# Performance work log

Hardware: AMD Instinct MI355X
Metric: run time of the kernel (lower is better)

The kernel has to match this reference:

```python
import jax, jax.numpy as jnp
import numpy as np

N_NODES = 100000
FEAT_DIM = 128
EMBED_DIM = 128
NUM_SAMPLE = 10


def setup_inputs() -> dict:
    key = jax.random.key(0)
    k1, k2, k3, k4, k5 = jax.random.split(key, 5)
    features = jax.random.normal(k1, (N_NODES, FEAT_DIM), dtype=jnp.float32)
    W1 = jax.random.normal(k2, (EMBED_DIM, FEAT_DIM), dtype=jnp.float32) * (1.0 / np.sqrt(FEAT_DIM))
    W2 = jax.random.normal(k3, (EMBED_DIM, EMBED_DIM), dtype=jnp.float32) * (1.0 / np.sqrt(EMBED_DIM))
    adj = jax.random.randint(k4, (N_NODES, NUM_SAMPLE), 0, N_NODES, dtype=jnp.int64)
    nodes = jax.random.randint(k5, (N_NODES,), 0, N_NODES, dtype=jnp.int64)
    return {"features": features, "W1": W1, "W2": W2, "adj": adj, "nodes": nodes}


def reference(features, W1, W2, adj, nodes):
    # 2-layer GraphSAGE with gcn=True: mean over {self} U sampled neighbors,
    # then relu(agg @ W.T). Layer 1 is computed for all nodes since layer 2
    # needs embeddings of arbitrary neighbors.
    n = features.shape[0]
    self_idx = jnp.arange(n, dtype=adj.dtype)[:, None]            # [N,1]
    neigh1 = jnp.concatenate([self_idx, adj], axis=1)             # [N,S+1]
    agg1 = jnp.mean(features[neigh1], axis=1)                     # [N,F] (gather+mean)
    h1 = jax.nn.relu(agg1 @ W1.T)                                 # [N,E]

    neigh2 = jnp.concatenate([nodes[:, None], adj[nodes]], axis=1)  # [B,S+1]
    agg2 = jnp.mean(h1[neigh2], axis=1)                           # [B,E]
    out = jax.nn.relu(agg2 @ W2.T).T                              # [E,B], Encoder returns embed_dim x num_nodes
    return out
```

## Files before the change

kernel.cpp:

```cpp
#include <hip/hip_runtime.h>

#define N_NODES 100000
#define DIM 128
#define NS 10
#define SCALE (1.0f / 11.0f)

typedef unsigned int uint;
typedef unsigned short ushort;
typedef __attribute__((ext_vector_type(8))) short bf16x8;
typedef __attribute__((ext_vector_type(4))) float f32x4;

__device__ inline float bl(uint u) {
    union { uint x; float f; } c; c.x = u << 16; return c.f;
}
__device__ inline uint f2b(float x) {
    union { float f; uint u; } c; c.f = x;
    return (c.u + 0x7FFFu + ((c.u >> 16) & 1u)) >> 16;
}

__global__ __launch_bounds__(256) void wsplit(const float* __restrict__ W1,
                                              const float* __restrict__ W2,
                                              ushort* __restrict__ o) {
    const int i = blockIdx.x * 256 + threadIdx.x;
    const float a = W1[i];
    uint h = f2b(a);
    o[i] = (ushort)h;
    o[16384 + i] = (ushort)f2b(a - bl(h));
    const float b = W2[i];
    h = f2b(b);
    o[32768 + i] = (ushort)h;
    o[49152 + i] = (ushort)f2b(b - bl(h));
}

__global__ __launch_bounds__(256, 2) void gemm1(const float* __restrict__ X,
                                                const ushort* __restrict__ Whi,
                                                const ushort* __restrict__ Wlo,
                                                ushort* __restrict__ C) {
    __shared__ __align__(16) ushort lds[8192];
    const int t = threadIdx.x;
    const int lane = t & 63;
    const int wave = t >> 6;
    const int m16 = lane & 15;
    const int kq = lane >> 4;
    const int r0 = blockIdx.x * 32;

    const int v0 = t, v1 = t + 256;
    const int ln0 = v0 & 63, ln1 = v1 & 63;
    const float* s0 = X + (size_t)(r0 + (v0 >> 8) * 16 + (ln0 & 15)) * DIM +
                      ((v0 >> 6) & 3) * 32 + (ln0 >> 4) * 8;
    const float* s1 = X + (size_t)(r0 + (v1 >> 8) * 16 + (ln1 & 15)) * DIM +
                      ((v1 >> 6) & 3) * 32 + (ln1 >> 4) * 8;
    const float4 f00 = *(const float4*)(s0);
    const float4 f01 = *(const float4*)(s0 + 4);
    const float4 f10 = *(const float4*)(s1);
    const float4 f11 = *(const float4*)(s1 + 4);

    bf16x8 wh[2][4], wl[2][4];
#pragma unroll
    for (int c = 0; c < 2; ++c)
#pragma unroll
        for (int ks = 0; ks < 4; ++ks) {
            const size_t off = (size_t)((2 * wave + c) * 16 + m16) * DIM + ks * 32 + kq * 8;
            wh[c][ks] = *(const bf16x8*)(Whi + off);
            wl[c][ks] = *(const bf16x8*)(Wlo + off);
        }

    {
        const float xs[8] = {f00.x, f00.y, f00.z, f00.w, f01.x, f01.y, f01.z, f01.w};
        bf16x8 hi, lo;
#pragma unroll
        for (int j = 0; j < 8; ++j) {
            const uint hb = f2b(xs[j]);
            hi[j] = (short)hb;
            lo[j] = (short)f2b(xs[j] - bl(hb));
        }
        *(bf16x8*)(lds + (v0 >> 6) * 512 + ln0 * 8) = hi;
        *(bf16x8*)(lds + 4096 + (v0 >> 6) * 512 + ln0 * 8) = lo;
    }
    {
        const float xs[8] = {f10.x, f10.y, f10.z, f10.w, f11.x, f11.y, f11.z, f11.w};
        bf16x8 hi, lo;
#pragma unroll
        for (int j = 0; j < 8; ++j) {
            const uint hb = f2b(xs[j]);
            hi[j] = (short)hb;
            lo[j] = (short)f2b(xs[j] - bl(hb));
        }
        *(bf16x8*)(lds + (v1 >> 6) * 512 + ln1 * 8) = hi;
        *(bf16x8*)(lds + 4096 + (v1 >> 6) * 512 + ln1 * 8) = lo;
    }
    __syncthreads();

    f32x4 acc[2][2];
#pragma unroll
    for (int bt = 0; bt < 2; ++bt)
#pragma unroll
        for (int c = 0; c < 2; ++c) acc[bt][c] = (f32x4){0.f, 0.f, 0.f, 0.f};

#pragma unroll
    for (int ks = 0; ks < 4; ++ks) {
#pragma unroll
        for (int bt = 0; bt < 2; ++bt) {
            const int g = bt * 4 + ks;
            const bf16x8 xh = *(const bf16x8*)(lds + g * 512 + lane * 8);
            const bf16x8 xl = *(const bf16x8*)(lds + 4096 + g * 512 + lane * 8);
#pragma unroll
            for (int c = 0; c < 2; ++c) {
                acc[bt][c] = __builtin_amdgcn_mfma_f32_16x16x32_bf16(wh[c][ks], xh, acc[bt][c], 0, 0, 0);
                acc[bt][c] = __builtin_amdgcn_mfma_f32_16x16x32_bf16(wl[c][ks], xh, acc[bt][c], 0, 0, 0);
                acc[bt][c] = __builtin_amdgcn_mfma_f32_16x16x32_bf16(wh[c][ks], xl, acc[bt][c], 0, 0, 0);
            }
        }
    }

#pragma unroll
    for (int bt = 0; bt < 2; ++bt) {
        const size_t row = (size_t)(r0 + bt * 16 + m16);
#pragma unroll
        for (int c = 0; c < 2; ++c) {
            uint2 w;
            w.x = f2b(acc[bt][c][0]) | (f2b(acc[bt][c][1]) << 16);
            w.y = f2b(acc[bt][c][2]) | (f2b(acc[bt][c][3]) << 16);
            *(uint2*)(C + row * DIM + (2 * wave + c) * 16 + kq * 4) = w;
        }
    }
}

__global__ __launch_bounds__(256, 2) void gemm2t(const ushort* __restrict__ P,
                                                 const ushort* __restrict__ Whi,
                                                 const ushort* __restrict__ Wlo,
                                                 float* __restrict__ out) {
    __shared__ __align__(16) ushort lds[4096];
    const int t = threadIdx.x;
    const int lane = t & 63;
    const int wave = t >> 6;
    const int m16 = lane & 15;
    const int kq = lane >> 4;
    const int r0 = blockIdx.x * 32;

    const int v0 = t, v1 = t + 256;
    const int ln0 = v0 & 63, ln1 = v1 & 63;
    const ushort* s0 = P + (size_t)(r0 + (v0 >> 8) * 16 + (ln0 & 15)) * DIM +
                       ((v0 >> 6) & 3) * 32 + (ln0 >> 4) * 8;
    const ushort* s1 = P + (size_t)(r0 + (v1 >> 8) * 16 + (ln1 & 15)) * DIM +
                       ((v1 >> 6) & 3) * 32 + (ln1 >> 4) * 8;
    const bf16x8 p0 = *(const bf16x8*)(s0);
    const bf16x8 p1 = *(const bf16x8*)(s1);

    bf16x8 wh[2][4], wl[2][4];
#pragma unroll
    for (int c = 0; c < 2; ++c)
#pragma unroll
        for (int ks = 0; ks < 4; ++ks) {
            const size_t off = (size_t)((2 * wave + c) * 16 + m16) * DIM + ks * 32 + kq * 8;
            wh[c][ks] = *(const bf16x8*)(Whi + off);
            wl[c][ks] = *(const bf16x8*)(Wlo + off);
        }

    *(bf16x8*)(lds + (v0 >> 6) * 512 + ln0 * 8) = p0;
    *(bf16x8*)(lds + (v1 >> 6) * 512 + ln1 * 8) = p1;
    __syncthreads();

    f32x4 acc[2][2];
#pragma unroll
    for (int bt = 0; bt < 2; ++bt)
#pragma unroll
        for (int c = 0; c < 2; ++c) acc[bt][c] = (f32x4){0.f, 0.f, 0.f, 0.f};

#pragma unroll
    for (int ks = 0; ks < 4; ++ks) {
#pragma unroll
        for (int bt = 0; bt < 2; ++bt) {
            const bf16x8 pa = *(const bf16x8*)(lds + (bt * 4 + ks) * 512 + lane * 8);
#pragma unroll
            for (int c = 0; c < 2; ++c) {
                acc[bt][c] = __builtin_amdgcn_mfma_f32_16x16x32_bf16(pa, wh[c][ks], acc[bt][c], 0, 0, 0);
                acc[bt][c] = __builtin_amdgcn_mfma_f32_16x16x32_bf16(pa, wl[c][ks], acc[bt][c], 0, 0, 0);
            }
        }
    }

#pragma unroll
    for (int bt = 0; bt < 2; ++bt) {
        const int b = r0 + bt * 16 + kq * 4;
#pragma unroll
        for (int c = 0; c < 2; ++c) {
            const int e = (2 * wave + c) * 16 + m16;
            float4 v;
            v.x = fmaxf(acc[bt][c][0], 0.f);
            v.y = fmaxf(acc[bt][c][1], 0.f);
            v.z = fmaxf(acc[bt][c][2], 0.f);
            v.w = fmaxf(acc[bt][c][3], 0.f);
            *(float4*)(out + (size_t)e * N_NODES + b) = v;
        }
    }
}

__global__ __launch_bounds__(256) void agg1(const ushort* __restrict__ FW,
                                            const int* __restrict__ adj,
                                            ushort* __restrict__ H) {
    const int t = threadIdx.x;
    const int team = t >> 5;
    const int j = t & 31;
    const int i = blockIdx.x * 8 + team;
    int av = 0;
    if (j < NS) av = adj[(size_t)i * NS + j];
    const uint2 x = ((const uint2*)(FW + (size_t)i * DIM))[j];
    float a0 = bl(x.x), a1 = bl(x.x >> 16), a2 = bl(x.y), a3 = bl(x.y >> 16);
#pragma unroll
    for (int s = 0; s < NS; ++s) {
        const int idx = __shfl(av, s, 32);
        const uint2 u = ((const uint2*)(FW + (size_t)idx * DIM))[j];
        a0 += bl(u.x); a1 += bl(u.x >> 16); a2 += bl(u.y); a3 += bl(u.y >> 16);
    }
    a0 = fmaxf(a0 * SCALE, 0.f);
    a1 = fmaxf(a1 * SCALE, 0.f);
    a2 = fmaxf(a2 * SCALE, 0.f);
    a3 = fmaxf(a3 * SCALE, 0.f);
    uint2 w;
    w.x = f2b(a0) | (f2b(a1) << 16);
    w.y = f2b(a2) | (f2b(a3) << 16);
    ((uint2*)(H + (size_t)i * DIM))[j] = w;
}

__global__ __launch_bounds__(256) void agg2b(const ushort* __restrict__ H,
                                             const int* __restrict__ adj,
                                             const int* __restrict__ nodes,
                                             ushort* __restrict__ P) {
    const int t = threadIdx.x;
    const int team = t >> 5;
    const int j = t & 31;
    const int i = blockIdx.x * 8 + team;
    const int n = nodes[i];
    int av = 0;
    if (j < NS) av = adj[(size_t)n * NS + j];
    const uint2 x = ((const uint2*)(H + (size_t)n * DIM))[j];
    float a0 = bl(x.x), a1 = bl(x.x >> 16), a2 = bl(x.y), a3 = bl(x.y >> 16);
#pragma unroll
    for (int s = 0; s < NS; ++s) {
        const int idx = __shfl(av, s, 32);
        const uint2 u = ((const uint2*)(H + (size_t)idx * DIM))[j];
        a0 += bl(u.x); a1 += bl(u.x >> 16); a2 += bl(u.y); a3 += bl(u.y >> 16);
    }
    a0 *= SCALE; a1 *= SCALE; a2 *= SCALE; a3 *= SCALE;
    uint2 w;
    w.x = f2b(a0) | (f2b(a1) << 16);
    w.y = f2b(a2) | (f2b(a3) << 16);
    ((uint2*)(P + (size_t)i * DIM))[j] = w;
}

extern "C" void kernel_launch(void* const* d_in, const int* in_sizes, int n_in,
                              void* d_out, int out_size, void* d_ws, size_t ws_size,
                              hipStream_t stream) {
    const float* features = (const float*)d_in[0];
    const float* W1 = (const float*)d_in[1];
    const float* W2 = (const float*)d_in[2];
    const int* adj = (const int*)d_in[3];
    const int* nodes = (const int*)d_in[4];
    float* out = (float*)d_out;

    const size_t NE = (size_t)N_NODES * DIM;
    ushort* fw = (ushort*)d_ws;
    ushort* h1 = fw + NE;
    ushort* wpl = h1 + NE;
    ushort* w1hi = wpl;
    ushort* w1lo = wpl + 16384;
    ushort* w2hi = wpl + 32768;
    ushort* w2lo = wpl + 49152;

    wsplit<<<64, 256, 0, stream>>>(W1, W2, wpl);
    gemm1<<<N_NODES / 32, 256, 0, stream>>>(features, w1hi, w1lo, fw);
    agg1<<<N_NODES / 8, 256, 0, stream>>>(fw, adj, h1);
    agg2b<<<N_NODES / 8, 256, 0, stream>>>(h1, adj, nodes, fw);
    gemm2t<<<N_NODES / 32, 256, 0, stream>>>(fw, w2hi, w2lo, out);
}
```

Before: 153.6 us.

## Fuse layer-2 aggregation into GEMM2 and widen gather loads in agg1

The layer-2 neighbor gather and mean are folded into the second GEMM kernel. The aggregated rows are written straight into LDS in MFMA operand layout, so the intermediate P buffer no longer makes a round trip through global memory, and one launch is removed. Both aggregation paths now use 16-byte loads with 16-thread teams covering two rows each. All 11 gathers are issued up front and neighbor indices are staged in LDS, which is meant to raise memory-level parallelism. In exchange there are more registers per thread and a serial two-level index lookup (nodes, then adj) inside the GEMM block before the gathers can start.

```diff
diff --git a/kernel.cpp b/kernel.cpp
--- a/kernel.cpp
+++ b/kernel.cpp
@@ -126,39 +126,105 @@
     }
 }
 
-__global__ __launch_bounds__(256, 2) void gemm2t(const ushort* __restrict__ P,
+__global__ __launch_bounds__(256) void agg1(const ushort* __restrict__ FW,
+                                            const int* __restrict__ adj,
+                                            ushort* __restrict__ H) {
+    __shared__ int idx_lds[320];
+    const int t = threadIdx.x;
+    const int r0 = blockIdx.x * 32;
+    for (int l = t; l < 320; l += 256)
+        idx_lds[l] = adj[(size_t)r0 * NS + l];
+    __syncthreads();
+    const int team = t >> 4;
+    const int j = t & 15;
+#pragma unroll
+    for (int rp = 0; rp < 2; ++rp) {
+        const int ri = team * 2 + rp;
+        const int row = r0 + ri;
+        uint4 u[11];
+        u[0] = *(const uint4*)(FW + (size_t)row * DIM + j * 8);
+#pragma unroll
+        for (int s = 0; s < NS; ++s)
+            u[1 + s] = *(const uint4*)(FW + (size_t)idx_lds[ri * NS + s] * DIM + j * 8);
+        float a[8];
+#pragma unroll
+        for (int k = 0; k < 8; ++k) a[k] = 0.f;
+#pragma unroll
+        for (int s = 0; s < 11; ++s) {
+            a[0] += bl(u[s].x); a[1] += bl(u[s].x >> 16);
+            a[2] += bl(u[s].y); a[3] += bl(u[s].y >> 16);
+            a[4] += bl(u[s].z); a[5] += bl(u[s].z >> 16);
+            a[6] += bl(u[s].w); a[7] += bl(u[s].w >> 16);
+        }
+        uint4 w;
+        w.x = f2b(fmaxf(a[0] * SCALE, 0.f)) | (f2b(fmaxf(a[1] * SCALE, 0.f)) << 16);
+        w.y = f2b(fmaxf(a[2] * SCALE, 0.f)) | (f2b(fmaxf(a[3] * SCALE, 0.f)) << 16);
+        w.z = f2b(fmaxf(a[4] * SCALE, 0.f)) | (f2b(fmaxf(a[5] * SCALE, 0.f)) << 16);
+        w.w = f2b(fmaxf(a[6] * SCALE, 0.f)) | (f2b(fmaxf(a[7] * SCALE, 0.f)) << 16);
+        *(uint4*)(H + (size_t)row * DIM + j * 8) = w;
+    }
+}
+
+__global__ __launch_bounds__(256, 2) void gemm2f(const ushort* __restrict__ H,
+                                                 const int* __restrict__ adj,
+                                                 const int* __restrict__ nodes,
                                                  const ushort* __restrict__ Whi,
                                                  const ushort* __restrict__ Wlo,
                                                  float* __restrict__ out) {
-    __shared__ __align__(16) ushort lds[4096];
+    __shared__ __align__(16) ushort plds[4096];
+    __shared__ int idx_lds[32 * 11];
     const int t = threadIdx.x;
     const int lane = t & 63;
     const int wave = t >> 6;
-    const int m16 = lane & 15;
+    const int m16w = lane & 15;
     const int kq = lane >> 4;
     const int r0 = blockIdx.x * 32;
 
-    const int v0 = t, v1 = t + 256;
-    const int ln0 = v0 & 63, ln1 = v1 & 63;
-    const ushort* s0 = P + (size_t)(r0 + (v0 >> 8) * 16 + (ln0 & 15)) * DIM +
-                       ((v0 >> 6) & 3) * 32 + (ln0 >> 4) * 8;
-    const ushort* s1 = P + (size_t)(r0 + (v1 >> 8) * 16 + (ln1 & 15)) * DIM +
-                       ((v1 >> 6) & 3) * 32 + (ln1 >> 4) * 8;
-    const bf16x8 p0 = *(const bf16x8*)(s0);
-    const bf16x8 p1 = *(const bf16x8*)(s1);
+    if (t < 32) idx_lds[t * 11] = nodes[r0 + t];
 
     bf16x8 wh[2][4], wl[2][4];
 #pragma unroll
     for (int c = 0; c < 2; ++c)
 #pragma unroll
         for (int ks = 0; ks < 4; ++ks) {
-            const size_t off = (size_t)((2 * wave + c) * 16 + m16) * DIM + ks * 32 + kq * 8;
+            const size_t off = (size_t)((2 * wave + c) * 16 + m16w) * DIM + ks * 32 + kq * 8;
             wh[c][ks] = *(const bf16x8*)(Whi + off);
             wl[c][ks] = *(const bf16x8*)(Wlo + off);
         }
-
-    *(bf16x8*)(lds + (v0 >> 6) * 512 + ln0 * 8) = p0;
-    *(bf16x8*)(lds + (v1 >> 6) * 512 + ln1 * 8) = p1;
+    __syncthreads();
+    for (int l = t; l < 320; l += 256) {
+        const int bi = l / 10;
+        const int s = l - bi * 10;
+        idx_lds[bi * 11 + 1 + s] = adj[(size_t)idx_lds[bi * 11] * NS + s];
+    }
+    __syncthreads();
+
+    const int team = t >> 4;
+    const int j = t & 15;
+#pragma unroll
+    for (int rp = 0; rp < 2; ++rp) {
+        const int ri = team * 2 + rp;
+        uint4 u[11];
+#pragma unroll
+        for (int s = 0; s < 11; ++s)
+            u[s] = *(const uint4*)(H + (size_t)idx_lds[ri * 11 + s] * DIM + j * 8);
+        float a[8];
+#pragma unroll
+        for (int k = 0; k < 8; ++k) a[k] = 0.f;
+#pragma unroll
+        for (int s = 0; s < 11; ++s) {
+            a[0] += bl(u[s].x); a[1] += bl(u[s].x >> 16);
+            a[2] += bl(u[s].y); a[3] += bl(u[s].y >> 16);
+            a[4] += bl(u[s].z); a[5] += bl(u[s].z >> 16);
+            a[6] += bl(u[s].w); a[7] += bl(u[s].w >> 16);
+        }
+        bf16x8 pw;
+#pragma unroll
+        for (int k = 0; k < 8; ++k) pw[k] = (short)f2b(a[k] * SCALE);
+        const int bt = ri >> 4;
+        const int m16 = ri & 15;
+        *(bf16x8*)(plds + (bt * 4 + (j >> 2)) * 512 + ((j & 3) * 16 + m16) * 8) = pw;
+    }
     __syncthreads();
 
     f32x4 acc[2][2];
@@ -171,7 +237,7 @@
     for (int ks = 0; ks < 4; ++ks) {
 #pragma unroll
         for (int bt = 0; bt < 2; ++bt) {
-            const bf16x8 pa = *(const bf16x8*)(lds + (bt * 4 + ks) * 512 + lane * 8);
+            const bf16x8 pa = *(const bf16x8*)(plds + (bt * 4 + ks) * 512 + lane * 8);
 #pragma unroll
             for (int c = 0; c < 2; ++c) {
                 acc[bt][c] = __builtin_amdgcn_mfma_f32_16x16x32_bf16(pa, wh[c][ks], acc[bt][c], 0, 0, 0);
@@ -185,7 +251,7 @@
         const int b = r0 + bt * 16 + kq * 4;
 #pragma unroll
         for (int c = 0; c < 2; ++c) {
-            const int e = (2 * wave + c) * 16 + m16;
+            const int e = (2 * wave + c) * 16 + m16w;
             float4 v;
             v.x = fmaxf(acc[bt][c][0], 0.f);
             v.y = fmaxf(acc[bt][c][1], 0.f);
@@ -194,59 +260,6 @@
             *(float4*)(out + (size_t)e * N_NODES + b) = v;
         }
     }
-}
-
-__global__ __launch_bounds__(256) void agg1(const ushort* __restrict__ FW,
-                                            const int* __restrict__ adj,
-                                            ushort* __restrict__ H) {
-    const int t = threadIdx.x;
-    const int team = t >> 5;
-    const int j = t & 31;
-    const int i = blockIdx.x * 8 + team;
-    int av = 0;
-    if (j < NS) av = adj[(size_t)i * NS + j];
-    const uint2 x = ((const uint2*)(FW + (size_t)i * DIM))[j];
-    float a0 = bl(x.x), a1 = bl(x.x >> 16), a2 = bl(x.y), a3 = bl(x.y >> 16);
-#pragma unroll
-    for (int s = 0; s < NS; ++s) {
-        const int idx = __shfl(av, s, 32);
-        const uint2 u = ((const uint2*)(FW + (size_t)idx * DIM))[j];
-        a0 += bl(u.x); a1 += bl(u.x >> 16); a2 += bl(u.y); a3 += bl(u.y >> 16);
-    }
-    a0 = fmaxf(a0 * SCALE, 0.f);
-    a1 = fmaxf(a1 * SCALE, 0.f);
-    a2 = fmaxf(a2 * SCALE, 0.f);
-    a3 = fmaxf(a3 * SCALE, 0.f);
-    uint2 w;
-    w.x = f2b(a0) | (f2b(a1) << 16);
-    w.y = f2b(a2) | (f2b(a3) << 16);
-    ((uint2*)(H + (size_t)i * DIM))[j] = w;
-}
-
-__global__ __launch_bounds__(256) void agg2b(const ushort* __restrict__ H,
-                                             const int* __restrict__ adj,
-                                             const int* __restrict__ nodes,
-                                             ushort* __restrict__ P) {
-    const int t = threadIdx.x;
-    const int team = t >> 5;
-    const int j = t & 31;
-    const int i = blockIdx.x * 8 + team;
-    const int n = nodes[i];
-    int av = 0;
-    if (j < NS) av = adj[(size_t)n * NS + j];
-    const uint2 x = ((const uint2*)(H + (size_t)n * DIM))[j];
-    float a0 = bl(x.x), a1 = bl(x.x >> 16), a2 = bl(x.y), a3 = bl(x.y >> 16);
-#pragma unroll
-    for (int s = 0; s < NS; ++s) {
-        const int idx = __shfl(av, s, 32);
-        const uint2 u = ((const uint2*)(H + (size_t)idx * DIM))[j];
-        a0 += bl(u.x); a1 += bl(u.x >> 16); a2 += bl(u.y); a3 += bl(u.y >> 16);
-    }
-    a0 *= SCALE; a1 *= SCALE; a2 *= SCALE; a3 *= SCALE;
-    uint2 w;
-    w.x = f2b(a0) | (f2b(a1) << 16);
-    w.y = f2b(a2) | (f2b(a3) << 16);
-    ((uint2*)(P + (size_t)i * DIM))[j] = w;
 }
 
 extern "C" void kernel_launch(void* const* d_in, const int* in_sizes, int n_in,
@@ -270,7 +283,6 @@
 
     wsplit<<<64, 256, 0, stream>>>(W1, W2, wpl);
     gemm1<<<N_NODES / 32, 256, 0, stream>>>(features, w1hi, w1lo, fw);
-    agg1<<<N_NODES / 8, 256, 0, stream>>>(fw, adj, h1);
-    agg2b<<<N_NODES / 8, 256, 0, stream>>>(h1, adj, nodes, fw);
-    gemm2t<<<N_NODES / 32, 256, 0, stream>>>(fw, w2hi, w2lo, out);
-}
+    agg1<<<N_NODES / 32, 256, 0, stream>>>(fw, adj, h1);
+    gemm2f<<<N_NODES / 32, 256, 0, stream>>>(h1, adj, nodes, w2hi, w2lo, out);
+}
```

Measured after the change: 144.9 us. 1.06x faster.
